# Optimization experiments

Hardware: AMD Instinct MI355X
Metric: run time of the kernel (lower is better)

## Reference

```python
import jax, jax.numpy as jnp
import numpy as np

N = 100_000   # nodes
E = 1_200_000 # edges
D = 64        # in_dim
H = 64        # hidden_dim
B = 1000      # graphs in batch
C = 10        # num_classes
TOPO = 64     # topo_dim
BN_EPS = 1e-5


def setup_inputs() -> dict:
    key = jax.random.key(0)
    ks = jax.random.split(key, 24)
    x = jax.random.normal(ks[0], (N, D), dtype=jnp.float32)
    edge_index = jax.random.randint(ks[1], (2, E), 0, N, dtype=jnp.int32)
    # sorted graph ids; force last id = B-1 so batch.max()+1 == B (matches torch path)
    batch = jnp.sort(jax.random.randint(ks[2], (N,), 0, B, dtype=jnp.int32)).at[-1].set(B - 1)
    topo = jax.random.normal(ks[3], (B, TOPO), dtype=jnp.float32)
    s = 0.05
    return {
        "x": x, "edge_index": edge_index, "batch": batch, "topo": topo,
        # conv1 MLP: Linear(D,H) -> BN(H) -> ReLU -> Linear(H,H) -> ReLU
        "W1a": jax.random.normal(ks[4], (D, H)) * s, "b1a": jax.random.normal(ks[5], (H,)) * s,
        "g1": 1.0 + jax.random.normal(ks[6], (H,)) * s, "be1": jax.random.normal(ks[7], (H,)) * s,
        "m1": jax.random.normal(ks[8], (H,)) * s, "v1": 0.5 + jax.random.uniform(ks[9], (H,)),
        "W1b": jax.random.normal(ks[10], (H, H)) * s, "b1b": jax.random.normal(ks[11], (H,)) * s,
        # conv2 MLP: Linear(H,H) -> BN(H) -> ReLU
        "W2": jax.random.normal(ks[12], (H, H)) * s, "b2": jax.random.normal(ks[13], (H,)) * s,
        "g2": 1.0 + jax.random.normal(ks[14], (H,)) * s, "be2": jax.random.normal(ks[15], (H,)) * s,
        "m2": jax.random.normal(ks[16], (H,)) * s, "v2": 0.5 + jax.random.uniform(ks[17], (H,)),
        # topo_net: Linear(TOPO,H) -> ReLU
        "Wt": jax.random.normal(ks[18], (TOPO, H)) * s, "bt": jax.random.normal(ks[19], (H,)) * s,
        # classifier: Linear(2H, C)
        "Wc": jax.random.normal(ks[20], (2 * H, C)) * s, "bc": jax.random.normal(ks[21], (C,)) * s,
    }


def _bn_eval(v, g, b, m, var):
    # BatchNorm1d in eval mode: affine with running stats
    return g * (v - m) * jax.lax.rsqrt(var + BN_EPS) + b


def _gin_agg(h, src, dst):
    # GINConv (eps=0): (1+eps)*x_i + sum_{j->i} x_j ; scatter-add over dst
    return h + jax.ops.segment_sum(h[src], dst, num_segments=N)


def reference(x, edge_index, batch, topo,
              W1a, b1a, g1, be1, m1, v1, W1b, b1b,
              W2, b2, g2, be2, m2, v2, Wt, bt, Wc, bc):
    src, dst = edge_index[0], edge_index[1]
    # conv1: MLP(agg(x)) = Lin -> BN -> ReLU -> Lin -> ReLU; outer relu from forward
    h = _gin_agg(x, src, dst)                              # [N, D]
    h = jax.nn.relu(_bn_eval(h @ W1a + b1a, g1, be1, m1, v1))
    h = jax.nn.relu(h @ W1b + b1b)                         # [N, H]
    h = jax.nn.relu(h)                                     # F.relu(conv1(...))
    # dropout(p=0.5) is identity in eval mode
    # conv2: Lin -> BN -> ReLU, then outer relu
    h = _gin_agg(h, src, dst)                              # [N, H]
    h = jax.nn.relu(_bn_eval(h @ W2 + b2, g2, be2, m2, v2))
    h = jax.nn.relu(h)
    # global_add_pool: sum nodes per graph
    x_struct = jax.ops.segment_sum(h, batch, num_segments=B)   # [B, H]
    # topo already [B, TOPO] => all reshape/pad branches are no-ops
    x_topo = jax.nn.relu(topo @ Wt + bt)                   # [B, H]
    combined = jnp.concatenate([x_struct, x_topo], axis=1) # [B, 2H]
    return combined @ Wc + bc                              # [B, C]
```

## Files before the change

kernel.cpp:

```cpp
#include <hip/hip_runtime.h>

#define N_NODES 100000
#define N_EDGES 1200000
#define DIM     64
#define BGRAPHS 1000
#define NCLASS  10
#define BN_EPS  1e-5f

#define NBUCK   256
#define NPB     391
#define MAGIC   10984572u
#define CHUNK   8192
#define NBLK_P  147
#define CAP     8192
#define NB_C    3125

typedef __attribute__((ext_vector_type(8))) short   bfx8;
typedef __attribute__((ext_vector_type(4))) float   f32x4;
typedef __attribute__((ext_vector_type(8))) unsigned short u16x8;

__device__ __forceinline__ unsigned short f2bf(float f) {
    unsigned u = __builtin_bit_cast(unsigned, f);
    unsigned r = (u + 0x7FFFu + ((u >> 16) & 1u)) >> 16;
    return (unsigned short)r;
}
__device__ __forceinline__ float bf2f(unsigned short h) {
    unsigned u = ((unsigned)h) << 16;
    return __builtin_bit_cast(float, u);
}

__global__ __launch_bounds__(256) void convhist_kernel(
    const float* __restrict__ x, unsigned short* __restrict__ xb,
    float* __restrict__ xs, const int* __restrict__ ei,
    int* __restrict__ gpart) {
    __shared__ int cnt[NBUCK];
    int t = threadIdx.x;
    if (blockIdx.x < NBLK_P) {
        int blk = blockIdx.x;
        cnt[t] = 0;
        __syncthreads();
        int e0 = blk * CHUNK;
        for (int i = t; i < CHUNK; i += 256) {
            int e = e0 + i;
            if (e >= N_EDGES) break;
            unsigned d = (unsigned)ei[N_EDGES + e];
            atomicAdd(&cnt[__umulhi(d, MAGIC)], 1);
        }
        __syncthreads();
        gpart[blk * NBUCK + t] = cnt[t];
    } else {
        int i = (blockIdx.x - NBLK_P) * 256 + t;
        const int n8 = N_NODES * DIM / 8;
        if (i < n8) {
            float4 a = ((const float4*)x)[i * 2];
            float4 b = ((const float4*)x)[i * 2 + 1];
            u16x8 o;
            o[0] = f2bf(a.x); o[1] = f2bf(a.y); o[2] = f2bf(a.z); o[3] = f2bf(a.w);
            o[4] = f2bf(b.x); o[5] = f2bf(b.y); o[6] = f2bf(b.z); o[7] = f2bf(b.w);
            ((u16x8*)xb)[i] = o;
        }
        if (i < BGRAPHS * DIM) xs[i] = 0.f;
    }
}

__global__ __launch_bounds__(256) void scanB_kernel(const int* __restrict__ gpart,
                                                    int* __restrict__ base,
                                                    int* __restrict__ cursor) {
    __shared__ int tmp[256];
    int t = threadIdx.x;
    int s = 0;
    for (int blk = 0; blk < NBLK_P; ++blk) s += gpart[blk * NBUCK + t];
    tmp[t] = s;
    __syncthreads();
    for (int off = 1; off < 256; off <<= 1) {
        int a = (t >= off) ? tmp[t - off] : 0;
        __syncthreads();
        tmp[t] += a;
        __syncthreads();
    }
    int excl = tmp[t] - s;
    base[t] = excl;
    cursor[t] = excl;
    if (t == 255) base[256] = N_EDGES;
}

__global__ __launch_bounds__(256) void part_kernel(const int* __restrict__ ei,
                                                   int* __restrict__ cursor,
                                                   int* __restrict__ srcbuf,
                                                   unsigned short* __restrict__ dstlbuf) {
    __shared__ int cnt[NBUCK];
    __shared__ int cur[NBUCK];
    int t = threadIdx.x, blk = blockIdx.x;
    cnt[t] = 0;
    __syncthreads();
    int e0 = blk * CHUNK;
    for (int i = t; i < CHUNK; i += 256) {
        int e = e0 + i;
        if (e >= N_EDGES) break;
        unsigned d = (unsigned)ei[N_EDGES + e];
        atomicAdd(&cnt[__umulhi(d, MAGIC)], 1);
    }
    __syncthreads();
    cur[t] = atomicAdd(&cursor[t], cnt[t]);
    __syncthreads();
    for (int i = t; i < CHUNK; i += 256) {
        int e = e0 + i;
        if (e >= N_EDGES) break;
        unsigned d = (unsigned)ei[N_EDGES + e];
        int s = ei[e];
        int b = __umulhi(d, MAGIC);
        int pos = atomicAdd(&cur[b], 1);
        srcbuf[pos] = s;
        dstlbuf[pos] = (unsigned short)(d - b * NPB);
    }
}

__global__ __launch_bounds__(256) void refine_kernel(const int* __restrict__ srcbuf,
                                                     const unsigned short* __restrict__ dstlbuf,
                                                     const int* __restrict__ base,
                                                     int* __restrict__ csr_src,
                                                     int* __restrict__ rowptr) {
    __shared__ int cnt[NPB + 1];
    __shared__ int cur[NPB + 1];
    __shared__ int tmp[256];
    __shared__ int outb[CAP];
    int t = threadIdx.x, b = blockIdx.x;
    int beg = base[b];
    int end = base[b + 1];

    for (int i = t; i < NPB + 1; i += 256) cnt[i] = 0;
    __syncthreads();
    for (int i = beg + t; i < end; i += 256)
        atomicAdd(&cnt[dstlbuf[i]], 1);
    __syncthreads();

    int i0 = 2 * t, i1 = 2 * t + 1;
    int v0 = (i0 < NPB) ? cnt[i0] : 0;
    int v1 = (i1 < NPB) ? cnt[i1] : 0;
    int s = v0 + v1;
    tmp[t] = s;
    __syncthreads();
    for (int off = 1; off < 256; off <<= 1) {
        int a = (t >= off) ? tmp[t - off] : 0;
        __syncthreads();
        tmp[t] += a;
        __syncthreads();
    }
    int excl = tmp[t] - s;
    if (i0 < NPB) cur[i0] = excl;
    if (i1 < NPB) cur[i1] = excl + v0;
    {
        int g0 = b * NPB + i0;
        if (i0 < NPB && g0 < N_NODES) rowptr[g0] = beg + excl;
        int g1 = b * NPB + i1;
        if (i1 < NPB && g1 < N_NODES) rowptr[g1] = beg + excl + v0;
    }
    if (b == NBUCK - 1 && t == 0) rowptr[N_NODES] = N_EDGES;
    __syncthreads();

    for (int i = beg + t; i < end; i += 256) {
        int dl = dstlbuf[i];
        int pos = atomicAdd(&cur[dl], 1);
        if (pos < CAP) outb[pos] = srcbuf[i];
    }
    __syncthreads();

    int nb = end - beg; if (nb > CAP) nb = CAP;
    for (int i = t; i < nb; i += 256) csr_src[beg + i] = outb[i];
}

__global__ __launch_bounds__(256) void gather_kernel(const unsigned short* __restrict__ feat,
                                                     const int* __restrict__ rowptr,
                                                     const int* __restrict__ csr_src,
                                                     unsigned short* __restrict__ out) {
    int t = threadIdx.x;
    int node = blockIdx.x * 32 + (t >> 3);
    int q = t & 7;
    if (node >= N_NODES) return;
    const u16x8* f8 = (const u16x8*)feat;
    u16x8 sv = f8[(long long)node * 8 + q];
    float acc[8];
    #pragma unroll
    for (int j = 0; j < 8; ++j) acc[j] = bf2f(sv[j]);
    int beg = rowptr[node], end = rowptr[node + 1];
    int k = beg;
    for (; k + 4 <= end; k += 4) {
        int s0 = csr_src[k], s1 = csr_src[k + 1];
        int s2 = csr_src[k + 2], s3 = csr_src[k + 3];
        u16x8 v0 = f8[(long long)s0 * 8 + q];
        u16x8 v1 = f8[(long long)s1 * 8 + q];
        u16x8 v2 = f8[(long long)s2 * 8 + q];
        u16x8 v3 = f8[(long long)s3 * 8 + q];
        #pragma unroll
        for (int j = 0; j < 8; ++j) acc[j] += bf2f(v0[j]);
        #pragma unroll
        for (int j = 0; j < 8; ++j) acc[j] += bf2f(v1[j]);
        #pragma unroll
        for (int j = 0; j < 8; ++j) acc[j] += bf2f(v2[j]);
        #pragma unroll
        for (int j = 0; j < 8; ++j) acc[j] += bf2f(v3[j]);
    }
    for (; k < end; ++k) {
        int sc = csr_src[k];
        u16x8 v = f8[(long long)sc * 8 + q];
        #pragma unroll
        for (int j = 0; j < 8; ++j) acc[j] += bf2f(v[j]);
    }
    u16x8 o;
    #pragma unroll
    for (int j = 0; j < 8; ++j) o[j] = f2bf(acc[j]);
    ((u16x8*)out)[(long long)node * 8 + q] = o;
}

__device__ __forceinline__ bfx8 load_wfrag(const float* __restrict__ W, int kt, int q, int col) {
    bfx8 f;
    #pragma unroll
    for (int j = 0; j < 8; ++j)
        f[j] = (short)f2bf(W[(kt * 32 + q * 8 + j) * 64 + col]);
    return f;
}

__global__ __launch_bounds__(256) void mlp1_kernel(
    const unsigned short* __restrict__ h0,
    const float* __restrict__ W1a, const float* __restrict__ b1a,
    const float* __restrict__ g1,  const float* __restrict__ be1,
    const float* __restrict__ m1,  const float* __restrict__ v1,
    const float* __restrict__ W1b, const float* __restrict__ b1b,
    unsigned short* __restrict__ h2) {
    __shared__ unsigned short h1t[4][16 * 72];
    __shared__ unsigned short outt[4][16 * 64];

    int t = threadIdx.x;
    int w = t >> 6, lane = t & 63;
    int m = lane & 15, q = lane >> 4;
    int row0 = blockIdx.x * 64 + w * 16;

    bfx8 wa[4][2], wb[4][2];
    #pragma unroll
    for (int nt = 0; nt < 4; ++nt) {
        #pragma unroll
        for (int kt = 0; kt < 2; ++kt) {
            wa[nt][kt] = load_wfrag(W1a, kt, q, nt * 16 + m);
            wb[nt][kt] = load_wfrag(W1b, kt, q, nt * 16 + m);
        }
    }
    float A1[4], B1[4], B2c[4];
    #pragma unroll
    for (int nt = 0; nt < 4; ++nt) {
        int c = nt * 16 + m;
        float s = g1[c] * rsqrtf(v1[c] + BN_EPS);
        A1[nt] = s;
        B1[nt] = b1a[c] * s + (be1[c] - m1[c] * s);
        B2c[nt] = b1b[c];
    }

    int rowA = row0 + m;
    if (rowA > N_NODES - 1) rowA = N_NODES - 1;
    const bfx8* ap = (const bfx8*)(h0 + (long long)rowA * 64);
    bfx8 a0 = ap[q];
    bfx8 a1 = ap[4 + q];
    f32x4 acc[4];
    #pragma unroll
    for (int nt = 0; nt < 4; ++nt) {
        acc[nt] = (f32x4){0.f, 0.f, 0.f, 0.f};
        acc[nt] = __builtin_amdgcn_mfma_f32_16x16x32_bf16(a0, wa[nt][0], acc[nt], 0, 0, 0);
        acc[nt] = __builtin_amdgcn_mfma_f32_16x16x32_bf16(a1, wa[nt][1], acc[nt], 0, 0, 0);
    }
    #pragma unroll
    for (int nt = 0; nt < 4; ++nt)
        #pragma unroll
        for (int r = 0; r < 4; ++r) {
            float v = fmaxf(acc[nt][r] * A1[nt] + B1[nt], 0.f);
            h1t[w][(q * 4 + r) * 72 + nt * 16 + m] = f2bf(v);
        }
    __syncthreads();

    const bfx8* hp = (const bfx8*)&h1t[w][m * 72];
    bfx8 c0 = hp[q];
    bfx8 c1 = hp[4 + q];
    f32x4 acc2[4];
    #pragma unroll
    for (int nt = 0; nt < 4; ++nt) {
        acc2[nt] = (f32x4){0.f, 0.f, 0.f, 0.f};
        acc2[nt] = __builtin_amdgcn_mfma_f32_16x16x32_bf16(c0, wb[nt][0], acc2[nt], 0, 0, 0);
        acc2[nt] = __builtin_amdgcn_mfma_f32_16x16x32_bf16(c1, wb[nt][1], acc2[nt], 0, 0, 0);
    }
    #pragma unroll
    for (int nt = 0; nt < 4; ++nt)
        #pragma unroll
        for (int r = 0; r < 4; ++r) {
            float v = fmaxf(acc2[nt][r] + B2c[nt], 0.f);
            outt[w][(q * 4 + r) * 64 + nt * 16 + m] = f2bf(v);
        }
    __syncthreads();

    #pragma unroll
    for (int i = lane; i < 128; i += 64) {
        int rr = i >> 3, cc = i & 7;
        int rg = row0 + rr;
        if (rg < N_NODES)
            ((float4*)h2)[(long long)rg * 8 + cc] = *(const float4*)&outt[w][rr * 64 + cc * 8];
    }
}

__global__ __launch_bounds__(256) void mlp2_kernel(
    const unsigned short* __restrict__ h3,
    const float* __restrict__ W2, const float* __restrict__ b2,
    const float* __restrict__ g2, const float* __restrict__ be2,
    const float* __restrict__ m2, const float* __restrict__ v2,
    const int* __restrict__ batch,
    float* __restrict__ xs) {
    __shared__ float pool[64 * 64];
    __shared__ int bts[64];

    int t = threadIdx.x;
    int w = t >> 6, lane = t & 63;
    int m = lane & 15, q = lane >> 4;
    int row0b = blockIdx.x * 64;
    int row0 = row0b + w * 16;

    bfx8 wf[4][2];
    #pragma unroll
    for (int nt = 0; nt < 4; ++nt)
        #pragma unroll
        for (int kt = 0; kt < 2; ++kt)
            wf[nt][kt] = load_wfrag(W2, kt, q, nt * 16 + m);
    float A[4], Bc[4];
    #pragma unroll
    for (int nt = 0; nt < 4; ++nt) {
        int c = nt * 16 + m;
        float s = g2[c] * rsqrtf(v2[c] + BN_EPS);
        A[nt] = s;
        Bc[nt] = b2[c] * s + (be2[c] - m2[c] * s);
    }
    if (t < 64) {
        int rg = row0b + t;
        bts[t] = (rg < N_NODES) ? batch[rg] : -1;
    }

    int rowA = row0 + m;
    if (rowA > N_NODES - 1) rowA = N_NODES - 1;
    const bfx8* ap = (const bfx8*)(h3 + (long long)rowA * 64);
    bfx8 a0 = ap[q];
    bfx8 a1 = ap[4 + q];
    f32x4 acc[4];
    #pragma unroll
    for (int nt = 0; nt < 4; ++nt) {
        acc[nt] = (f32x4){0.f, 0.f, 0.f, 0.f};
        acc[nt] = __builtin_amdgcn_mfma_f32_16x16x32_bf16(a0, wf[nt][0], acc[nt], 0, 0, 0);
        acc[nt] = __builtin_amdgcn_mfma_f32_16x16x32_bf16(a1, wf[nt][1], acc[nt], 0, 0, 0);
    }
    #pragma unroll
    for (int nt = 0; nt < 4; ++nt)
        #pragma unroll
        for (int r = 0; r < 4; ++r) {
            float v = fmaxf(acc[nt][r] * A[nt] + Bc[nt], 0.f);
            pool[(w * 16 + q * 4 + r) * 64 + nt * 16 + m] = v;
        }
    __syncthreads();

    int col = t & 63;
    int r0 = (t >> 6) * 16;
    int cb = bts[r0];
    float cur = 0.f;
    #pragma unroll
    for (int r = 0; r < 16; ++r) {
        int b = bts[r0 + r];
        if (b != cb) {
            if (cb >= 0) unsafeAtomicAdd(&xs[cb * 64 + col], cur);
            cb = b;
            cur = 0.f;
        }
        cur += pool[(r0 + r) * 64 + col];
    }
    if (cb >= 0) unsafeAtomicAdd(&xs[cb * 64 + col], cur);
}

__global__ __launch_bounds__(64) void head_kernel(
    const float* __restrict__ xs, const float* __restrict__ topo,
    const float* __restrict__ Wt, const float* __restrict__ bt,
    const float* __restrict__ Wc, const float* __restrict__ bc,
    float* __restrict__ out) {
    __shared__ float trow[64];
    __shared__ float comb[128];
    int b = blockIdx.x;
    int h = threadIdx.x;
    trow[h] = topo[b * 64 + h];
    __syncthreads();
    float acc = bt[h];
    #pragma unroll
    for (int k = 0; k < 64; ++k) acc += trow[k] * Wt[k * 64 + h];
    comb[h] = xs[b * 64 + h];
    comb[64 + h] = fmaxf(acc, 0.f);
    __syncthreads();
    if (h < NCLASS) {
        float o = bc[h];
        #pragma unroll
        for (int k = 0; k < 128; ++k) o += comb[k] * Wc[k * NCLASS + h];
        out[b * NCLASS + h] = o;
    }
}

extern "C" void kernel_launch(void* const* d_in, const int* in_sizes, int n_in,
                              void* d_out, int out_size, void* d_ws, size_t ws_size,
                              hipStream_t stream) {
    const float* x     = (const float*)d_in[0];
    const int*   ei    = (const int*)d_in[1];
    const int*   batch = (const int*)d_in[2];
    const float* topo  = (const float*)d_in[3];
    const float* W1a   = (const float*)d_in[4];
    const float* b1a   = (const float*)d_in[5];
    const float* g1    = (const float*)d_in[6];
    const float* be1   = (const float*)d_in[7];
    const float* m1    = (const float*)d_in[8];
    const float* v1    = (const float*)d_in[9];
    const float* W1b   = (const float*)d_in[10];
    const float* b1b   = (const float*)d_in[11];
    const float* W2    = (const float*)d_in[12];
    const float* b2    = (const float*)d_in[13];
    const float* g2    = (const float*)d_in[14];
    const float* be2   = (const float*)d_in[15];
    const float* m2    = (const float*)d_in[16];
    const float* v2    = (const float*)d_in[17];
    const float* Wt    = (const float*)d_in[18];
    const float* bt    = (const float*)d_in[19];
    const float* Wc    = (const float*)d_in[20];
    const float* bc    = (const float*)d_in[21];
    float* out = (float*)d_out;

    char* p = (char*)d_ws;
    unsigned short* xbf  = (unsigned short*)p; p += (size_t)N_NODES * DIM * 2;
    unsigned short* bufA = (unsigned short*)p; p += (size_t)N_NODES * DIM * 2;
    unsigned short* bufB = (unsigned short*)p; p += (size_t)N_NODES * DIM * 2;
    float* xs      = (float*)p; p += (size_t)BGRAPHS * DIM * 4;
    int*   rowptr  = (int*)p;   p += (size_t)(N_NODES + 16) * 4;
    int*   gpart   = (int*)p;   p += (size_t)NBLK_P * NBUCK * 4;
    int*   base    = (int*)p;   p += 1040;
    int*   cursor  = (int*)p;   p += 1024;
    int*   srcbuf  = (int*)p;   p += (size_t)N_EDGES * 4;
    unsigned short* dstlbuf = (unsigned short*)p; p += (size_t)N_EDGES * 2;
    int*   csr_src = (int*)p;

    convhist_kernel<<<NBLK_P + NB_C, 256, 0, stream>>>(x, xbf, xs, ei, gpart);
    scanB_kernel<<<1, 256, 0, stream>>>(gpart, base, cursor);
    part_kernel<<<NBLK_P, 256, 0, stream>>>(ei, cursor, srcbuf, dstlbuf);
    refine_kernel<<<NBUCK, 256, 0, stream>>>(srcbuf, dstlbuf, base, csr_src, rowptr);
    gather_kernel<<<(N_NODES + 31) / 32, 256, 0, stream>>>(xbf, rowptr, csr_src, bufA);
    mlp1_kernel<<<(N_NODES + 63) / 64, 256, 0, stream>>>(
        bufA, W1a, b1a, g1, be1, m1, v1, W1b, b1b, bufB);
    gather_kernel<<<(N_NODES + 31) / 32, 256, 0, stream>>>(bufB, rowptr, csr_src, bufA);
    mlp2_kernel<<<(N_NODES + 63) / 64, 256, 0, stream>>>(
        bufA, W2, b2, g2, be2, m2, v2, batch, xs);
    head_kernel<<<BGRAPHS, 64, 0, stream>>>(xs, topo, Wt, bt, Wc, bc, out);
}
```

Before: 252.9 us.

## Balance edge work across threads in gather via block-level edge splitting

The gather kernel now splits the block's 32 nodes' combined edge range evenly across the 32 thread groups instead of assigning one node per group. Each group walks its slice and flushes partial sums into a shared-memory fp32 accumulator with atomics whenever it crosses a node boundary. The aim is to remove load imbalance from variable node degree. The cost is shared-memory atomics, a binary search, and the loss of the 4-way unrolled load batching, so fewer memory loads are in flight per thread.

```diff
diff --git a/kernel.cpp b/kernel.cpp
--- a/kernel.cpp
+++ b/kernel.cpp
@@ -173,43 +173,63 @@
                                                      const int* __restrict__ rowptr,
                                                      const int* __restrict__ csr_src,
                                                      unsigned short* __restrict__ out) {
+    __shared__ float accf[32 * 65];
+    __shared__ int rp[33];
     int t = threadIdx.x;
-    int node = blockIdx.x * 32 + (t >> 3);
+    int node = t >> 3;
     int q = t & 7;
-    if (node >= N_NODES) return;
+    int n0 = blockIdx.x * 32;
     const u16x8* f8 = (const u16x8*)feat;
-    u16x8 sv = f8[(long long)node * 8 + q];
-    float acc[8];
-    #pragma unroll
-    for (int j = 0; j < 8; ++j) acc[j] = bf2f(sv[j]);
-    int beg = rowptr[node], end = rowptr[node + 1];
-    int k = beg;
-    for (; k + 4 <= end; k += 4) {
-        int s0 = csr_src[k], s1 = csr_src[k + 1];
-        int s2 = csr_src[k + 2], s3 = csr_src[k + 3];
-        u16x8 v0 = f8[(long long)s0 * 8 + q];
-        u16x8 v1 = f8[(long long)s1 * 8 + q];
-        u16x8 v2 = f8[(long long)s2 * 8 + q];
-        u16x8 v3 = f8[(long long)s3 * 8 + q];
-        #pragma unroll
-        for (int j = 0; j < 8; ++j) acc[j] += bf2f(v0[j]);
-        #pragma unroll
-        for (int j = 0; j < 8; ++j) acc[j] += bf2f(v1[j]);
-        #pragma unroll
-        for (int j = 0; j < 8; ++j) acc[j] += bf2f(v2[j]);
-        #pragma unroll
-        for (int j = 0; j < 8; ++j) acc[j] += bf2f(v3[j]);
-    }
-    for (; k < end; ++k) {
-        int sc = csr_src[k];
-        u16x8 v = f8[(long long)sc * 8 + q];
-        #pragma unroll
-        for (int j = 0; j < 8; ++j) acc[j] += bf2f(v[j]);
-    }
+
+    if (t < 33) rp[t] = rowptr[n0 + t];
+    {
+        u16x8 sv = f8[(long long)(n0 + node) * 8 + q];
+        #pragma unroll
+        for (int j = 0; j < 8; ++j) accf[node * 65 + q * 8 + j] = bf2f(sv[j]);
+    }
+    __syncthreads();
+
+    int beg = rp[0], end = rp[32];
+    int len = end - beg;
+    int chunk = (len + 31) >> 5;
+    int rb = beg + node * chunk;
+    int re = rb + chunk; if (re > end) re = end;
+    if (rb < re) {
+        int lo = 0, hi = 31;
+        while (lo < hi) { int mid = (lo + hi + 1) >> 1; if (rp[mid] <= rb) lo = mid; else hi = mid - 1; }
+        int ni = lo;
+        float acc[8];
+        #pragma unroll
+        for (int j = 0; j < 8; ++j) acc[j] = 0.f;
+        int ne = 0;
+        for (int k = rb; k < re; ++k) {
+            while (k >= rp[ni + 1]) {
+                if (ne) {
+                    #pragma unroll
+                    for (int j = 0; j < 8; ++j) atomicAdd(&accf[ni * 65 + q * 8 + j], acc[j]);
+                    #pragma unroll
+                    for (int j = 0; j < 8; ++j) acc[j] = 0.f;
+                    ne = 0;
+                }
+                ++ni;
+            }
+            int sc = csr_src[k];
+            u16x8 v = f8[(long long)sc * 8 + q];
+            #pragma unroll
+            for (int j = 0; j < 8; ++j) acc[j] += bf2f(v[j]);
+            ++ne;
+        }
+        if (ne) {
+            #pragma unroll
+            for (int j = 0; j < 8; ++j) atomicAdd(&accf[ni * 65 + q * 8 + j], acc[j]);
+        }
+    }
+    __syncthreads();
+
     u16x8 o;
     #pragma unroll
-    for (int j = 0; j < 8; ++j) o[j] = f2bf(acc[j]);
-    ((u16x8*)out)[(long long)node * 8 + q] = o;
+    for (int j = 0; j < 8; ++j) o[j] = f2bf(accf[node * 65 + q * 8 + j]);
+    ((u16x8*)out)[(long long)(n0 + node) * 8 + q] = o;
 }
 
 __device__ __forceinline__ bfx8 load_wfrag(const float* __restrict__ W, int kt, int q, int col) {
@@ -445,10 +465,10 @@
     scanB_kernel<<<1, 256, 0, stream>>>(gpart, base, cursor);
     part_kernel<<<NBLK_P, 256, 0, stream>>>(ei, cursor, srcbuf, dstlbuf);
     refine_kernel<<<NBUCK, 256, 0, stream>>>(srcbuf, dstlbuf, base, csr_src, rowptr);
-    gather_kernel<<<(N_NODES + 31) / 32, 256, 0, stream>>>(xbf, rowptr, csr_src, bufA);
+    gather_kernel<<<N_NODES / 32, 256, 0, stream>>>(xbf, rowptr, csr_src, bufA);
     mlp1_kernel<<<(N_NODES + 63) / 64, 256, 0, stream>>>(
         bufA, W1a, b1a, g1, be1, m1, v1, W1b, b1b, bufB);
-    gather_kernel<<<(N_NODES + 31) / 32, 256, 0, stream>>>(bufB, rowptr, csr_src, bufA);
+    gather_kernel<<<N_NODES / 32, 256, 0, stream>>>(bufB, rowptr, csr_src, bufA);
     mlp2_kernel<<<(N_NODES + 63) / 64, 256, 0, stream>>>(
         bufA, W2, b2, g2, be2, m2, v2, batch, xs);
     head_kernel<<<BGRAPHS, 64, 0, stream>>>(xs, topo, Wt, bt, Wc, bc, out);
```

Result: slower. 348.0 us (+37.6%).

## Replace CSR refine and gather with bucketed LDS atomic scatter aggregation

Applied to the files above, without the earlier changes.

Drops the refine kernel that built a full CSR (rowptr plus sorted csr_src) and the per-node gather kernel. Aggregation now runs directly on the bucket-partitioned edge list: each block takes one bucket of 391 destination nodes and half of the feature columns, seeds an LDS fp32 accumulator with the self features, and atomically adds gathered source rows into LDS. This saves one kernel launch and the CSR write and read traffic. In exchange it uses only 512 blocks, adds heavy LDS float atomic contention, and makes the summation order nondeterministic.

```diff
diff --git a/kernel.cpp b/kernel.cpp
--- a/kernel.cpp
+++ b/kernel.cpp
@@ -12,7 +12,6 @@
 #define MAGIC   10984572u
 #define CHUNK   8192
 #define NBLK_P  147
-#define CAP     8192
 #define NB_C    3125
 
 typedef __attribute__((ext_vector_type(8))) short   bfx8;
@@ -115,101 +114,50 @@
     }
 }
 
-__global__ __launch_bounds__(256) void refine_kernel(const int* __restrict__ srcbuf,
-                                                     const unsigned short* __restrict__ dstlbuf,
-                                                     const int* __restrict__ base,
-                                                     int* __restrict__ csr_src,
-                                                     int* __restrict__ rowptr) {
-    __shared__ int cnt[NPB + 1];
-    __shared__ int cur[NPB + 1];
-    __shared__ int tmp[256];
-    __shared__ int outb[CAP];
-    int t = threadIdx.x, b = blockIdx.x;
-    int beg = base[b];
-    int end = base[b + 1];
-
-    for (int i = t; i < NPB + 1; i += 256) cnt[i] = 0;
-    __syncthreads();
-    for (int i = beg + t; i < end; i += 256)
-        atomicAdd(&cnt[dstlbuf[i]], 1);
-    __syncthreads();
-
-    int i0 = 2 * t, i1 = 2 * t + 1;
-    int v0 = (i0 < NPB) ? cnt[i0] : 0;
-    int v1 = (i1 < NPB) ? cnt[i1] : 0;
-    int s = v0 + v1;
-    tmp[t] = s;
-    __syncthreads();
-    for (int off = 1; off < 256; off <<= 1) {
-        int a = (t >= off) ? tmp[t - off] : 0;
-        __syncthreads();
-        tmp[t] += a;
-        __syncthreads();
-    }
-    int excl = tmp[t] - s;
-    if (i0 < NPB) cur[i0] = excl;
-    if (i1 < NPB) cur[i1] = excl + v0;
-    {
-        int g0 = b * NPB + i0;
-        if (i0 < NPB && g0 < N_NODES) rowptr[g0] = beg + excl;
-        int g1 = b * NPB + i1;
-        if (i1 < NPB && g1 < N_NODES) rowptr[g1] = beg + excl + v0;
-    }
-    if (b == NBUCK - 1 && t == 0) rowptr[N_NODES] = N_EDGES;
-    __syncthreads();
-
-    for (int i = beg + t; i < end; i += 256) {
+__global__ __launch_bounds__(256) void scatter_kernel(
+    const unsigned short* __restrict__ feat,
+    const int* __restrict__ base,
+    const int* __restrict__ srcbuf,
+    const unsigned short* __restrict__ dstlbuf,
+    unsigned short* __restrict__ out) {
+    __shared__ float accf[NPB * 33];
+    int t = threadIdx.x;
+    int b = blockIdx.x >> 1;
+    int half = blockIdx.x & 1;
+    int n0 = b * NPB;
+    int ql = t & 3, sg = t >> 2;
+    const u16x8* f8 = (const u16x8*)feat;
+
+    for (int nl = sg; nl < NPB; nl += 64) {
+        int g = n0 + nl;
+        if (g < N_NODES) {
+            u16x8 sv = f8[(long long)g * 8 + half * 4 + ql];
+            #pragma unroll
+            for (int j = 0; j < 8; ++j) accf[nl * 33 + ql * 8 + j] = bf2f(sv[j]);
+        }
+    }
+    __syncthreads();
+
+    int beg = base[b], end = base[b + 1];
+    for (int i = beg + sg; i < end; i += 64) {
+        int src = srcbuf[i];
         int dl = dstlbuf[i];
-        int pos = atomicAdd(&cur[dl], 1);
-        if (pos < CAP) outb[pos] = srcbuf[i];
-    }
-    __syncthreads();
-
-    int nb = end - beg; if (nb > CAP) nb = CAP;
-    for (int i = t; i < nb; i += 256) csr_src[beg + i] = outb[i];
-}
-
-__global__ __launch_bounds__(256) void gather_kernel(const unsigned short* __restrict__ feat,
-                                                     const int* __restrict__ rowptr,
-                                                     const int* __restrict__ csr_src,
-                                                     unsigned short* __restrict__ out) {
-    int t = threadIdx.x;
-    int node = blockIdx.x * 32 + (t >> 3);
-    int q = t & 7;
-    if (node >= N_NODES) return;
-    const u16x8* f8 = (const u16x8*)feat;
-    u16x8 sv = f8[(long long)node * 8 + q];
-    float acc[8];
-    #pragma unroll
-    for (int j = 0; j < 8; ++j) acc[j] = bf2f(sv[j]);
-    int beg = rowptr[node], end = rowptr[node + 1];
-    int k = beg;
-    for (; k + 4 <= end; k += 4) {
-        int s0 = csr_src[k], s1 = csr_src[k + 1];
-        int s2 = csr_src[k + 2], s3 = csr_src[k + 3];
-        u16x8 v0 = f8[(long long)s0 * 8 + q];
-        u16x8 v1 = f8[(long long)s1 * 8 + q];
-        u16x8 v2 = f8[(long long)s2 * 8 + q];
-        u16x8 v3 = f8[(long long)s3 * 8 + q];
-        #pragma unroll
-        for (int j = 0; j < 8; ++j) acc[j] += bf2f(v0[j]);
-        #pragma unroll
-        for (int j = 0; j < 8; ++j) acc[j] += bf2f(v1[j]);
-        #pragma unroll
-        for (int j = 0; j < 8; ++j) acc[j] += bf2f(v2[j]);
-        #pragma unroll
-        for (int j = 0; j < 8; ++j) acc[j] += bf2f(v3[j]);
-    }
-    for (; k < end; ++k) {
-        int sc = csr_src[k];
-        u16x8 v = f8[(long long)sc * 8 + q];
-        #pragma unroll
-        for (int j = 0; j < 8; ++j) acc[j] += bf2f(v[j]);
-    }
-    u16x8 o;
-    #pragma unroll
-    for (int j = 0; j < 8; ++j) o[j] = f2bf(acc[j]);
-    ((u16x8*)out)[(long long)node * 8 + q] = o;
+        u16x8 v = f8[(long long)src * 8 + half * 4 + ql];
+        #pragma unroll
+        for (int j = 0; j < 8; ++j)
+            atomicAdd(&accf[dl * 33 + ql * 8 + j], bf2f(v[j]));
+    }
+    __syncthreads();
+
+    for (int nl = sg; nl < NPB; nl += 64) {
+        int g = n0 + nl;
+        if (g < N_NODES) {
+            u16x8 o;
+            #pragma unroll
+            for (int j = 0; j < 8; ++j) o[j] = f2bf(accf[nl * 33 + ql * 8 + j]);
+            ((u16x8*)out)[(long long)g * 8 + half * 4 + ql] = o;
+        }
+    }
 }
 
 __device__ __forceinline__ bfx8 load_wfrag(const float* __restrict__ W, int kt, int q, int col) {
@@ -433,22 +381,19 @@
     unsigned short* bufA = (unsigned short*)p; p += (size_t)N_NODES * DIM * 2;
     unsigned short* bufB = (unsigned short*)p; p += (size_t)N_NODES * DIM * 2;
     float* xs      = (float*)p; p += (size_t)BGRAPHS * DIM * 4;
-    int*   rowptr  = (int*)p;   p += (size_t)(N_NODES + 16) * 4;
     int*   gpart   = (int*)p;   p += (size_t)NBLK_P * NBUCK * 4;
     int*   base    = (int*)p;   p += 1040;
     int*   cursor  = (int*)p;   p += 1024;
     int*   srcbuf  = (int*)p;   p += (size_t)N_EDGES * 4;
-    unsigned short* dstlbuf = (unsigned short*)p; p += (size_t)N_EDGES * 2;
-    int*   csr_src = (int*)p;
+    unsigned short* dstlbuf = (unsigned short*)p;
 
     convhist_kernel<<<NBLK_P + NB_C, 256, 0, stream>>>(x, xbf, xs, ei, gpart);
     scanB_kernel<<<1, 256, 0, stream>>>(gpart, base, cursor);
     part_kernel<<<NBLK_P, 256, 0, stream>>>(ei, cursor, srcbuf, dstlbuf);
-    refine_kernel<<<NBUCK, 256, 0, stream>>>(srcbuf, dstlbuf, base, csr_src, rowptr);
-    gather_kernel<<<(N_NODES + 31) / 32, 256, 0, stream>>>(xbf, rowptr, csr_src, bufA);
+    scatter_kernel<<<NBUCK * 2, 256, 0, stream>>>(xbf, base, srcbuf, dstlbuf, bufA);
     mlp1_kernel<<<(N_NODES + 63) / 64, 256, 0, stream>>>(
         bufA, W1a, b1a, g1, be1, m1, v1, W1b, b1b, bufB);
-    gather_kernel<<<(N_NODES + 31) / 32, 256, 0, stream>>>(bufB, rowptr, csr_src, bufA);
+    scatter_kernel<<<NBUCK * 2, 256, 0, stream>>>(bufB, base, srcbuf, dstlbuf, bufA);
     mlp2_kernel<<<(N_NODES + 63) / 64, 256, 0, stream>>>(
         bufA, W2, b2, g2, be2, m2, v2, batch, xs);
     head_kernel<<<BGRAPHS, 64, 0, stream>>>(xs, topo, Wt, bt, Wc, bc, out);
```

Measured after the change: 976.1 us. 3.86x slower.
